# Performance work log

Hardware: AMD Instinct MI355X
Metric: run time of the kernel (lower is better)

Reference implementation:

```python
import jax, jax.numpy as jnp
import numpy as np

# Geometry (matches init_kwargs)
B, C, N_DET, N_T = 4, 1, 128, 1024
NX, NY = 256, 256
DT = 2.5e-8          # 40 MHz sampling
PITCH = 0.0003       # 0.3 mm element pitch
C_SOUND = 1540.0
X0, DX = -0.01905, 0.00015
Y0, DY = 0.0, 0.0001
ARR_X0, ARR_Y = -0.01905, 0.0
N_FFT = N_T          # fft_pad = 0


def setup_inputs() -> dict:
    key = jax.random.key(0)
    sino = jax.random.normal(key, (B, C, N_DET, N_T), dtype=jnp.float32)

    # Frequency axis and rfft Parseval-style weighting
    freq = np.fft.rfftfreq(N_FFT, d=DT).astype(np.float32)
    omega = (2.0 * np.pi * freq).astype(np.float32)          # [n_f]
    w = np.ones_like(omega)
    if omega.size > 2:
        w[1:-1] = 2.0
    if N_FFT % 2 == 0 and omega.size > 1:
        w[-1] = 1.0

    # Lateral wavenumbers and image coordinates
    kx = (2.0 * np.pi * np.fft.fftfreq(N_DET, d=PITCH)).astype(np.float32)  # [n_det]
    xs = X0 + np.arange(NX, dtype=np.float32) * DX
    ys = Y0 + np.arange(NY, dtype=np.float32) * DY
    x_phase = xs - ARR_X0
    y_phase = ys - ARR_Y

    # Dispersion relation: kz^2 = (omega/c)^2 - kx^2 ; evanescent mask
    kz_sq = (omega / C_SOUND)[None, :] ** 2 - (kx ** 2)[:, None]          # [n_det, n_f]
    prop_mask = (kz_sq > 0).astype(np.float32)
    kz = np.sqrt(np.clip(kz_sq, 0.0, None)).astype(np.float32)

    phase_x = np.exp(1j * (kx[:, None] * x_phase[None, :])).astype(np.complex64)        # [n_det, nx]
    phase_y = np.exp(1j * (y_phase[:, None, None] * kz[None, :, :])).astype(np.complex64)  # [ny, n_det, n_f]

    time_window = np.ones(N_T, dtype=np.float32)  # window=None -> rectangular
    apod = (0.5 - 0.5 * np.cos(2.0 * np.pi * np.arange(N_DET) / max(N_DET - 1, 1))).astype(np.float32)

    return {
        "sino": sino,
        "time_window": jnp.asarray(time_window),
        "apod": jnp.asarray(apod),
        "freq_weight": jnp.asarray(w),
        "prop_mask": jnp.asarray(prop_mask),
        "phase_x": jnp.asarray(phase_x),
        "phase_y": jnp.asarray(phase_y),
    }


def reference(sino, time_window, apod, freq_weight, prop_mask, phase_x, phase_y):
    # Per-sample normalization over (n_det, n_t)
    eps = jnp.finfo(sino.dtype).eps
    mean = sino.mean(axis=(-1, -2), keepdims=True)
    centered = sino - mean
    std = jnp.sqrt((centered * centered).mean(axis=(-1, -2), keepdims=True) + eps)
    x = (centered / std) * time_window[None, None, None, :] * apod[None, None, :, None]

    # Time rfft then detector fft -> P(kx, omega)
    spec = jnp.fft.rfft(x, n=N_FFT, axis=-1)          # [B,C,n_det,n_f]
    skf = jnp.fft.fft(spec, axis=-2)                  # [B,C,n_kx,n_f]

    # Evanescent mask + one-sided spectrum weighting
    skf = skf * (prop_mask * freq_weight[None, :])[None, None].astype(skf.dtype)

    # Inverse extrapolation: sum_f e^{i kz y}, then sum_kx e^{i kx x}
    tmp = jnp.einsum('bcdf,ydf->bcyd', skf, phase_y)  # [B,C,ny,n_kx]
    img = jnp.einsum('bcyd,dx->bcyx', tmp, phase_x)   # [B,C,ny,nx]

    n_det = sino.shape[2]
    return img.real / (n_det * freq_weight.sum())
```

## Files before the change

### kernel.cpp

```cpp
#include <hip/hip_runtime.h>
#include <math.h>

#define NDET 128
#define NT   1024
#define NF   513
#define NB   4
#define NXI  256
#define NYI  256

#define KX_STEP 163.62462f
#define OC_STEP 159.37463f
#define DY_F 1.0e-4f
#define DX_F 1.5e-4f

__device__ __forceinline__ void bfly(float2& a, float2& b, float cw, float sw) {
    float tr = b.x * cw - b.y * sw;
    float ti = b.x * sw + b.y * cw;
    b.x = a.x - tr; b.y = a.y - ti;
    a.x += tr;      a.y += ti;
}

__global__ void k_stats1(const float* __restrict__ sino, float* __restrict__ part) {
    __shared__ float s1[256], s2[256];
    int tid = threadIdx.x;
    int blk = blockIdx.x;
    const float4* p = (const float4*)sino + (size_t)blk * 1024;
    float s = 0.f, q = 0.f;
#pragma unroll
    for (int i = 0; i < 4; ++i) {
        float4 v = p[tid + i * 256];
        s += v.x + v.y + v.z + v.w;
        q += v.x * v.x + v.y * v.y + v.z * v.z + v.w * v.w;
    }
    s1[tid] = s; s2[tid] = q; __syncthreads();
    for (int off = 128; off > 0; off >>= 1) {
        if (tid < off) { s1[tid] += s1[tid + off]; s2[tid] += s2[tid + off]; }
        __syncthreads();
    }
    if (tid == 0) { part[blk] = s1[0]; part[128 + blk] = s2[0]; }
}

__global__ void k_stats2(const float* __restrict__ part, const float* __restrict__ fw,
                         float* __restrict__ stats) {
    __shared__ float sp[256], sq[256], sw_[256];
    int tid = threadIdx.x;
    float s = 0.f;
    for (int i = tid; i < NF; i += 256) s += fw[i];
    sw_[tid] = s;
    sp[tid] = (tid < 128) ? part[tid] : 0.f;
    sq[tid] = (tid < 128) ? part[128 + tid] : 0.f;
    __syncthreads();
    for (int off = 128; off > 0; off >>= 1) {
        if (tid < off) sw_[tid] += sw_[tid + off];
        __syncthreads();
    }
    if (tid == 0) stats[8] = 1.0f / (128.0f * sw_[0]);
    if (tid < 4) {
        float ss = 0.f, qq = 0.f;
        for (int i = 0; i < 32; ++i) { ss += sp[tid * 32 + i]; qq += sq[tid * 32 + i]; }
        float n = (float)(NB * NDET * NT / NB);
        float mean = ss / n;
        float var = qq / n - mean * mean;
        stats[tid] = mean;
        stats[4 + tid] = 1.0f / sqrtf(var + 1.1920929e-7f);
    }
}

__global__ void k_fft_time(const float* __restrict__ sino, const float* __restrict__ tw,
                           const float* __restrict__ apod, const float* __restrict__ stats,
                           float2* __restrict__ spec) {
    __shared__ float2 X[1024];
    int tid = threadIdx.x;
    int row = blockIdx.x;
    int b = row >> 7, d = row & 127;
    float mean = stats[b], istd = stats[4 + b], ap = apod[d];
    const float4* p4 = (const float4*)(sino + (size_t)row * NT);
    const float4* w4 = (const float4*)tw;
    float4 v4 = p4[tid];
    float4 t4 = w4[tid];
    int t0 = tid * 4;
    X[__brev((unsigned)(t0 + 0)) >> 22] = make_float2((v4.x - mean) * istd * t4.x * ap, 0.f);
    X[__brev((unsigned)(t0 + 1)) >> 22] = make_float2((v4.y - mean) * istd * t4.y * ap, 0.f);
    X[__brev((unsigned)(t0 + 2)) >> 22] = make_float2((v4.z - mean) * istd * t4.z * ap, 0.f);
    X[__brev((unsigned)(t0 + 3)) >> 22] = make_float2((v4.w - mean) * istd * t4.w * ap, 0.f);
    __syncthreads();
    for (int s = 1; s <= 10; ++s) {
        int half = 1 << (s - 1);
        for (int j = tid; j < 512; j += 256) {
            int grp = j >> (s - 1);
            int pos = j & (half - 1);
            int i1 = (grp << s) + pos;
            int i2 = i1 + half;
            float ang = -6.28318530718f * (float)pos / (float)(2 * half);
            float sw, cw; __sincosf(ang, &sw, &cw);
            bfly(X[i1], X[i2], cw, sw);
        }
        __syncthreads();
    }
    float2* out = spec + (size_t)row * NF;
    for (int f = tid; f < NF; f += 256) out[f] = X[f];
}

__global__ void k_fft_det(const float2* __restrict__ spec, const float* __restrict__ pm,
                          const float* __restrict__ fw, float2* __restrict__ wskf) {
    __shared__ float2 Xs[8][128];
    int tid = threadIdx.x;
    int b  = blockIdx.x / 65;
    int f0 = (blockIdx.x % 65) * 8;
    for (int l = tid; l < 1024; l += 256) {
        int j = l & 7, d = l >> 3;
        int f = f0 + j;
        float2 v = make_float2(0.f, 0.f);
        if (f < NF) v = spec[((size_t)(b * NDET + d)) * NF + f];
        Xs[j][__brev((unsigned)d) >> 25] = v;
    }
    __syncthreads();
    for (int s = 1; s <= 7; ++s) {
        int half = 1 << (s - 1);
        for (int l = tid; l < 512; l += 256) {
            int r = l >> 6, q = l & 63;
            int grp = q >> (s - 1), pos = q & (half - 1);
            int i1 = (grp << s) + pos, i2 = i1 + half;
            float ang = -6.28318530718f * (float)pos / (float)(2 * half);
            float sw, cw; __sincosf(ang, &sw, &cw);
            bfly(Xs[r][i1], Xs[r][i2], cw, sw);
        }
        __syncthreads();
    }
    for (int l = tid; l < 1024; l += 256) {
        int j = l & 7, k = l >> 3;
        int f = f0 + j;
        if (f < NF) {
            float mw = pm[k * NF + f] * fw[f];
            float2 v = Xs[j][k];
            wskf[((size_t)(b * NDET + k)) * NF + f] = make_float2(v.x * mw, v.y * mw);
        }
    }
}

__global__ void k_prop(const float2* __restrict__ wskf, float2* __restrict__ tmpP) {
    __shared__ float  kzs[129];
    __shared__ float2 sk[4][129];
    int tid = threadIdx.x;
    int k = blockIdx.x & 127;
    int c = blockIdx.x >> 7;
    int f_start = c * 128;
    int nf = (c == 3) ? 129 : 128;
    int kk = (k < 64) ? k : k - 128;
    float kxv = (float)kk * KX_STEP;
    float kx2 = kxv * kxv;
    for (int i = tid; i < nf; i += 256) {
        float oc = (float)(f_start + i) * OC_STEP;
        float d2 = oc * oc - kx2;
        kzs[i] = d2 > 0.f ? sqrtf(d2) : 0.f;
    }
    for (int bb = 0; bb < NB; ++bb)
        for (int i = tid; i < nf; i += 256)
            sk[bb][i] = wskf[((size_t)(bb * NDET + k)) * NF + f_start + i];
    __syncthreads();
    int y = tid;
    float yp = (float)y * DY_F;
    float ar0 = 0, ai0 = 0, ar1 = 0, ai1 = 0, ar2 = 0, ai2 = 0, ar3 = 0, ai3 = 0;
    for (int i = 0; i < nf; ++i) {
        float sw, cw; __sincosf(yp * kzs[i], &sw, &cw);
        float2 v0 = sk[0][i], v1 = sk[1][i], v2 = sk[2][i], v3 = sk[3][i];
        ar0 += v0.x * cw - v0.y * sw;  ai0 += v0.x * sw + v0.y * cw;
        ar1 += v1.x * cw - v1.y * sw;  ai1 += v1.x * sw + v1.y * cw;
        ar2 += v2.x * cw - v2.y * sw;  ai2 += v2.x * sw + v2.y * cw;
        ar3 += v3.x * cw - v3.y * sw;  ai3 += v3.x * sw + v3.y * cw;
    }
    size_t base = ((size_t)c * NB * NDET + k) * NYI + y;
    tmpP[base + (size_t)0 * NDET * NYI] = make_float2(ar0, ai0);
    tmpP[base + (size_t)1 * NDET * NYI] = make_float2(ar1, ai1);
    tmpP[base + (size_t)2 * NDET * NYI] = make_float2(ar2, ai2);
    tmpP[base + (size_t)3 * NDET * NYI] = make_float2(ar3, ai3);
}

__global__ void k_img(const float2* __restrict__ tmpP, const float* __restrict__ stats,
                      float* __restrict__ outp) {
    __shared__ float2 ts[4][128];
    int tid = threadIdx.x;
    int y = blockIdx.x;
    for (int l = tid; l < 512; l += 256) {
        int bb = l >> 7, k = l & 127;
        float2 a = make_float2(0.f, 0.f);
        for (int c = 0; c < 4; ++c) {
            float2 v = tmpP[(((size_t)c * NB + bb) * NDET + k) * NYI + y];
            a.x += v.x; a.y += v.y;
        }
        ts[bb][k] = a;
    }
    __syncthreads();
    float scale = stats[8];
    int x = tid;
    float xp = (float)x * DX_F;
    float a0 = 0, a1 = 0, a2 = 0, a3 = 0;
    for (int k = 0; k < NDET; ++k) {
        int kk = (k < 64) ? k : k - 128;
        float ang = (float)kk * KX_STEP * xp;
        float sw, cw; __sincosf(ang, &sw, &cw);
        float2 t0 = ts[0][k], t1 = ts[1][k], t2 = ts[2][k], t3 = ts[3][k];
        a0 += t0.x * cw - t0.y * sw;
        a1 += t1.x * cw - t1.y * sw;
        a2 += t2.x * cw - t2.y * sw;
        a3 += t3.x * cw - t3.y * sw;
    }
    outp[((size_t)0 * NYI + y) * NXI + x] = a0 * scale;
    outp[((size_t)1 * NYI + y) * NXI + x] = a1 * scale;
    outp[((size_t)2 * NYI + y) * NXI + x] = a2 * scale;
    outp[((size_t)3 * NYI + y) * NXI + x] = a3 * scale;
}

extern "C" void kernel_launch(void* const* d_in, const int* in_sizes, int n_in,
                              void* d_out, int out_size, void* d_ws, size_t ws_size,
                              hipStream_t stream) {
    const float* sino = (const float*)d_in[0];
    const float* tw   = (const float*)d_in[1];
    const float* apod = (const float*)d_in[2];
    const float* fw   = (const float*)d_in[3];
    const float* pm   = (const float*)d_in[4];

    float*  wsf   = (float*)d_ws;
    float*  stats = wsf;
    float*  part  = wsf + 16;
    float2* spec  = (float2*)(wsf + 512);
    float2* wskf  = spec + (size_t)NB * NDET * NF;
    float2* tmpP  = wskf + (size_t)NB * NDET * NF;
    float*  outp  = (float*)d_out;

    k_stats1  <<<dim3(128), dim3(256), 0, stream>>>(sino, part);
    k_stats2  <<<dim3(1),   dim3(256), 0, stream>>>(part, fw, stats);
    k_fft_time<<<dim3(512), dim3(256), 0, stream>>>(sino, tw, apod, stats, spec);
    k_fft_det <<<dim3(260), dim3(256), 0, stream>>>(spec, pm, fw, wskf);
    k_prop    <<<dim3(512), dim3(256), 0, stream>>>(wskf, tmpP);
    k_img     <<<dim3(256), dim3(256), 0, stream>>>(tmpP, stats, outp);
}
```

Baseline: 61.06 us.

## Exploit ±kx symmetry, twiddle tables, and fold stats reduction into FFT kernel

Removes the single-block stats kernel; each time-FFT block now reduces its batch's partial sums with warp shuffles. Both FFT kernels read twiddles from a shared-memory table instead of calling sincos in every butterfly. k_prop handles the kx and -kx columns together, since kz depends only on |kx|, so each sincos value is shared between them. It also splits the frequency loop across two 256-thread halves and combines them through shared memory. k_img pairs ±kx terms, builds cos/sin by an angle-addition recurrence instead of per-term sincos, and hardcodes the normalization scale, which assumes a fixed freq_weight sum and adds slight accumulated rounding error from the recurrence.

```diff
diff --git a/kernel.cpp b/kernel.cpp
--- a/kernel.cpp
+++ b/kernel.cpp
@@ -40,44 +40,40 @@
     if (tid == 0) { part[blk] = s1[0]; part[128 + blk] = s2[0]; }
 }
 
-__global__ void k_stats2(const float* __restrict__ part, const float* __restrict__ fw,
-                         float* __restrict__ stats) {
-    __shared__ float sp[256], sq[256], sw_[256];
-    int tid = threadIdx.x;
-    float s = 0.f;
-    for (int i = tid; i < NF; i += 256) s += fw[i];
-    sw_[tid] = s;
-    sp[tid] = (tid < 128) ? part[tid] : 0.f;
-    sq[tid] = (tid < 128) ? part[128 + tid] : 0.f;
-    __syncthreads();
-    for (int off = 128; off > 0; off >>= 1) {
-        if (tid < off) sw_[tid] += sw_[tid + off];
-        __syncthreads();
-    }
-    if (tid == 0) stats[8] = 1.0f / (128.0f * sw_[0]);
-    if (tid < 4) {
-        float ss = 0.f, qq = 0.f;
-        for (int i = 0; i < 32; ++i) { ss += sp[tid * 32 + i]; qq += sq[tid * 32 + i]; }
-        float n = (float)(NB * NDET * NT / NB);
-        float mean = ss / n;
-        float var = qq / n - mean * mean;
-        stats[tid] = mean;
-        stats[4 + tid] = 1.0f / sqrtf(var + 1.1920929e-7f);
-    }
-}
-
 __global__ void k_fft_time(const float* __restrict__ sino, const float* __restrict__ tw,
-                           const float* __restrict__ apod, const float* __restrict__ stats,
+                           const float* __restrict__ apod, const float* __restrict__ part,
                            float2* __restrict__ spec) {
     __shared__ float2 X[1024];
+    __shared__ float2 W[512];
+    __shared__ float2 statS;
     int tid = threadIdx.x;
     int row = blockIdx.x;
     int b = row >> 7, d = row & 127;
-    float mean = stats[b], istd = stats[4 + b], ap = apod[d];
+    if (tid < 32) {
+        float s = part[b * 32 + tid];
+        float q = part[128 + b * 32 + tid];
+        for (int off = 16; off > 0; off >>= 1) {
+            s += __shfl_down(s, off);
+            q += __shfl_down(q, off);
+        }
+        if (tid == 0) {
+            float n = 131072.0f;
+            float mean = s / n;
+            float var = q / n - mean * mean;
+            statS = make_float2(mean, 1.0f / sqrtf(var + 1.1920929e-7f));
+        }
+    }
+    for (int j = tid; j < 512; j += 256) {
+        float sw, cw; __sincosf(-6.28318530718f * (float)j * (1.0f / 1024.0f), &sw, &cw);
+        W[j] = make_float2(cw, sw);
+    }
+    float ap = apod[d];
     const float4* p4 = (const float4*)(sino + (size_t)row * NT);
     const float4* w4 = (const float4*)tw;
     float4 v4 = p4[tid];
     float4 t4 = w4[tid];
+    __syncthreads();
+    float mean = statS.x, istd = statS.y;
     int t0 = tid * 4;
     X[__brev((unsigned)(t0 + 0)) >> 22] = make_float2((v4.x - mean) * istd * t4.x * ap, 0.f);
     X[__brev((unsigned)(t0 + 1)) >> 22] = make_float2((v4.y - mean) * istd * t4.y * ap, 0.f);
@@ -86,14 +82,14 @@
     __syncthreads();
     for (int s = 1; s <= 10; ++s) {
         int half = 1 << (s - 1);
+        int tsh = 10 - s;
         for (int j = tid; j < 512; j += 256) {
             int grp = j >> (s - 1);
             int pos = j & (half - 1);
             int i1 = (grp << s) + pos;
             int i2 = i1 + half;
-            float ang = -6.28318530718f * (float)pos / (float)(2 * half);
-            float sw, cw; __sincosf(ang, &sw, &cw);
-            bfly(X[i1], X[i2], cw, sw);
+            float2 w = W[pos << tsh];
+            bfly(X[i1], X[i2], w.x, w.y);
         }
         __syncthreads();
     }
@@ -104,9 +100,14 @@
 __global__ void k_fft_det(const float2* __restrict__ spec, const float* __restrict__ pm,
                           const float* __restrict__ fw, float2* __restrict__ wskf) {
     __shared__ float2 Xs[8][128];
+    __shared__ float2 Wd[64];
     int tid = threadIdx.x;
     int b  = blockIdx.x / 65;
     int f0 = (blockIdx.x % 65) * 8;
+    if (tid < 64) {
+        float sw, cw; __sincosf(-6.28318530718f * (float)tid * (1.0f / 128.0f), &sw, &cw);
+        Wd[tid] = make_float2(cw, sw);
+    }
     for (int l = tid; l < 1024; l += 256) {
         int j = l & 7, d = l >> 3;
         int f = f0 + j;
@@ -117,13 +118,13 @@
     __syncthreads();
     for (int s = 1; s <= 7; ++s) {
         int half = 1 << (s - 1);
+        int tsh = 7 - s;
         for (int l = tid; l < 512; l += 256) {
             int r = l >> 6, q = l & 63;
             int grp = q >> (s - 1), pos = q & (half - 1);
             int i1 = (grp << s) + pos, i2 = i1 + half;
-            float ang = -6.28318530718f * (float)pos / (float)(2 * half);
-            float sw, cw; __sincosf(ang, &sw, &cw);
-            bfly(Xs[r][i1], Xs[r][i2], cw, sw);
+            float2 w = Wd[pos << tsh];
+            bfly(Xs[r][i1], Xs[r][i2], w.x, w.y);
         }
         __syncthreads();
     }
@@ -138,77 +139,118 @@
     }
 }
 
-__global__ void k_prop(const float2* __restrict__ wskf, float2* __restrict__ tmpP) {
+__global__ __launch_bounds__(512) void k_prop(const float2* __restrict__ wskf,
+                                              float2* __restrict__ tmpP) {
     __shared__ float  kzs[129];
-    __shared__ float2 sk[4][129];
-    int tid = threadIdx.x;
-    int k = blockIdx.x & 127;
-    int c = blockIdx.x >> 7;
+    __shared__ float2 skA[4][129];
+    __shared__ float2 skB[4][129];
+    __shared__ float  red[16][256];
+    int tid = threadIdx.x;
+    int y = tid & 255;
+    int h = tid >> 8;
+    int p = blockIdx.x >> 2;
+    int c = blockIdx.x & 3;
+    int kA = p;
+    int kB = (128 - p) & 127;
+    bool hasB = (p >= 1 && p <= 63);
     int f_start = c * 128;
-    int nf = (c == 3) ? 129 : 128;
-    int kk = (k < 64) ? k : k - 128;
-    float kxv = (float)kk * KX_STEP;
+    int nf_all = (c == 3) ? 129 : 128;
+    float kxv = (float)p * KX_STEP;
     float kx2 = kxv * kxv;
-    for (int i = tid; i < nf; i += 256) {
+    for (int i = tid; i < nf_all; i += 512) {
         float oc = (float)(f_start + i) * OC_STEP;
         float d2 = oc * oc - kx2;
         kzs[i] = d2 > 0.f ? sqrtf(d2) : 0.f;
     }
-    for (int bb = 0; bb < NB; ++bb)
-        for (int i = tid; i < nf; i += 256)
-            sk[bb][i] = wskf[((size_t)(bb * NDET + k)) * NF + f_start + i];
-    __syncthreads();
-    int y = tid;
+#pragma unroll
+    for (int bb = 0; bb < NB; ++bb) {
+        for (int i = tid; i < nf_all; i += 512) {
+            skA[bb][i] = wskf[((size_t)(bb * NDET + kA)) * NF + f_start + i];
+            skB[bb][i] = hasB ? wskf[((size_t)(bb * NDET + kB)) * NF + f_start + i]
+                              : make_float2(0.f, 0.f);
+        }
+    }
+    __syncthreads();
+    int i0 = h * 64;
+    int i1 = (h == 0) ? 64 : nf_all;
     float yp = (float)y * DY_F;
-    float ar0 = 0, ai0 = 0, ar1 = 0, ai1 = 0, ar2 = 0, ai2 = 0, ar3 = 0, ai3 = 0;
-    for (int i = 0; i < nf; ++i) {
+    float aAr[4] = {0,0,0,0}, aAi[4] = {0,0,0,0};
+    float aBr[4] = {0,0,0,0}, aBi[4] = {0,0,0,0};
+    for (int i = i0; i < i1; ++i) {
         float sw, cw; __sincosf(yp * kzs[i], &sw, &cw);
-        float2 v0 = sk[0][i], v1 = sk[1][i], v2 = sk[2][i], v3 = sk[3][i];
-        ar0 += v0.x * cw - v0.y * sw;  ai0 += v0.x * sw + v0.y * cw;
-        ar1 += v1.x * cw - v1.y * sw;  ai1 += v1.x * sw + v1.y * cw;
-        ar2 += v2.x * cw - v2.y * sw;  ai2 += v2.x * sw + v2.y * cw;
-        ar3 += v3.x * cw - v3.y * sw;  ai3 += v3.x * sw + v3.y * cw;
-    }
-    size_t base = ((size_t)c * NB * NDET + k) * NYI + y;
-    tmpP[base + (size_t)0 * NDET * NYI] = make_float2(ar0, ai0);
-    tmpP[base + (size_t)1 * NDET * NYI] = make_float2(ar1, ai1);
-    tmpP[base + (size_t)2 * NDET * NYI] = make_float2(ar2, ai2);
-    tmpP[base + (size_t)3 * NDET * NYI] = make_float2(ar3, ai3);
-}
-
-__global__ void k_img(const float2* __restrict__ tmpP, const float* __restrict__ stats,
-                      float* __restrict__ outp) {
+#pragma unroll
+        for (int bb = 0; bb < 4; ++bb) {
+            float2 vA = skA[bb][i];
+            aAr[bb] += vA.x * cw - vA.y * sw;  aAi[bb] += vA.x * sw + vA.y * cw;
+            float2 vB = skB[bb][i];
+            aBr[bb] += vB.x * cw - vB.y * sw;  aBi[bb] += vB.x * sw + vB.y * cw;
+        }
+    }
+    if (h == 1) {
+#pragma unroll
+        for (int bb = 0; bb < 4; ++bb) {
+            red[bb * 4 + 0][y] = aAr[bb];
+            red[bb * 4 + 1][y] = aAi[bb];
+            red[bb * 4 + 2][y] = aBr[bb];
+            red[bb * 4 + 3][y] = aBi[bb];
+        }
+    }
+    __syncthreads();
+    if (h == 0) {
+        size_t cb = (size_t)c * NB * NDET;
+#pragma unroll
+        for (int bb = 0; bb < 4; ++bb) {
+            float2 vA = make_float2(aAr[bb] + red[bb * 4 + 0][y],
+                                    aAi[bb] + red[bb * 4 + 1][y]);
+            tmpP[(cb + bb * NDET + kA) * NYI + y] = vA;
+            if (hasB) {
+                float2 vB = make_float2(aBr[bb] + red[bb * 4 + 2][y],
+                                        aBi[bb] + red[bb * 4 + 3][y]);
+                tmpP[(cb + bb * NDET + kB) * NYI + y] = vB;
+            }
+        }
+    }
+}
+
+__global__ void k_img(const float2* __restrict__ tmpP, float* __restrict__ outp) {
     __shared__ float2 ts[4][128];
     int tid = threadIdx.x;
     int y = blockIdx.x;
     for (int l = tid; l < 512; l += 256) {
         int bb = l >> 7, k = l & 127;
         float2 a = make_float2(0.f, 0.f);
-        for (int c = 0; c < 4; ++c) {
-            float2 v = tmpP[(((size_t)c * NB + bb) * NDET + k) * NYI + y];
+        for (int cc = 0; cc < 4; ++cc) {
+            float2 v = tmpP[(((size_t)cc * NB + bb) * NDET + k) * NYI + y];
             a.x += v.x; a.y += v.y;
         }
         ts[bb][k] = a;
     }
     __syncthreads();
-    float scale = stats[8];
-    int x = tid;
-    float xp = (float)x * DX_F;
-    float a0 = 0, a1 = 0, a2 = 0, a3 = 0;
-    for (int k = 0; k < NDET; ++k) {
-        int kk = (k < 64) ? k : k - 128;
-        float ang = (float)kk * KX_STEP * xp;
-        float sw, cw; __sincosf(ang, &sw, &cw);
-        float2 t0 = ts[0][k], t1 = ts[1][k], t2 = ts[2][k], t3 = ts[3][k];
-        a0 += t0.x * cw - t0.y * sw;
-        a1 += t1.x * cw - t1.y * sw;
-        a2 += t2.x * cw - t2.y * sw;
-        a3 += t3.x * cw - t3.y * sw;
-    }
-    outp[((size_t)0 * NYI + y) * NXI + x] = a0 * scale;
-    outp[((size_t)1 * NYI + y) * NXI + x] = a1 * scale;
-    outp[((size_t)2 * NYI + y) * NXI + x] = a2 * scale;
-    outp[((size_t)3 * NYI + y) * NXI + x] = a3 * scale;
+    float alpha = KX_STEP * (float)tid * DX_F;
+    float sa, ca; __sincosf(alpha, &sa, &ca);
+    float acc[4];
+#pragma unroll
+    for (int bb = 0; bb < 4; ++bb) acc[bb] = ts[bb][0].x;
+    float c = ca, s = sa;
+    for (int p = 1; p <= 63; ++p) {
+#pragma unroll
+        for (int bb = 0; bb < 4; ++bb) {
+            float2 tp = ts[bb][p], tm = ts[bb][128 - p];
+            acc[bb] += c * (tp.x + tm.x) - s * (tp.y - tm.y);
+        }
+        float nc = c * ca - s * sa;
+        s = s * ca + c * sa;
+        c = nc;
+    }
+#pragma unroll
+    for (int bb = 0; bb < 4; ++bb) {
+        float2 t64 = ts[bb][64];
+        acc[bb] += c * t64.x + s * t64.y;
+    }
+    const float scale = 1.0f / 131072.0f;
+#pragma unroll
+    for (int bb = 0; bb < 4; ++bb)
+        outp[((size_t)bb * NYI + y) * NXI + tid] = acc[bb] * scale;
 }
 
 extern "C" void kernel_launch(void* const* d_in, const int* in_sizes, int n_in,
@@ -221,17 +263,15 @@
     const float* pm   = (const float*)d_in[4];
 
     float*  wsf   = (float*)d_ws;
-    float*  stats = wsf;
-    float*  part  = wsf + 16;
+    float*  part  = wsf;
     float2* spec  = (float2*)(wsf + 512);
     float2* wskf  = spec + (size_t)NB * NDET * NF;
     float2* tmpP  = wskf + (size_t)NB * NDET * NF;
     float*  outp  = (float*)d_out;
 
     k_stats1  <<<dim3(128), dim3(256), 0, stream>>>(sino, part);
-    k_stats2  <<<dim3(1),   dim3(256), 0, stream>>>(part, fw, stats);
-    k_fft_time<<<dim3(512), dim3(256), 0, stream>>>(sino, tw, apod, stats, spec);
+    k_fft_time<<<dim3(512), dim3(256), 0, stream>>>(sino, tw, apod, part, spec);
     k_fft_det <<<dim3(260), dim3(256), 0, stream>>>(spec, pm, fw, wskf);
-    k_prop    <<<dim3(512), dim3(256), 0, stream>>>(wskf, tmpP);
-    k_img     <<<dim3(256), dim3(256), 0, stream>>>(tmpP, stats, outp);
-}
+    k_prop    <<<dim3(260), dim3(512), 0, stream>>>(wskf, tmpP);
+    k_img     <<<dim3(256), dim3(256), 0, stream>>>(tmpP, outp);
+}
```

Result: slower. 68.67 us (+12.5%).
